# Optimization experiments

Hardware: AMD Instinct MI355X
Metric: run time of the kernel (lower is better)

## Reference

```python
import jax, jax.numpy as jnp
import numpy as np

B, M, N, D, H = 4, 8, 128, 32, 64
SMALL_V = 1e-8


def setup_inputs() -> dict:
    key = jax.random.key(0)
    ks = jax.random.split(key, 12)
    s = 0.05
    x = jax.random.normal(ks[0], (B, M, N, D), jnp.float32)
    sizes = jax.random.randint(ks[1], (B,), N // 2, N + 1)
    valid = (jnp.arange(N)[None, :] < sizes[:, None]).astype(jnp.float32)  # [B,N]
    x = x * valid[:, None, :, None]  # zero out padded items
    return {
        "x": x,
        "x_size": sizes.astype(jnp.float32),
        "W1a": jax.random.normal(ks[2], (D, 2 * D), jnp.float32) * s,
        "b1a": jax.random.normal(ks[3], (2 * D,), jnp.float32) * s,
        "W1b": jax.random.normal(ks[4], (2 * D, D), jnp.float32) * s,
        "b1b": jax.random.normal(ks[5], (D,), jnp.float32) * s,
        "W2a": jax.random.normal(ks[6], (D, 2 * D), jnp.float32) * s,
        "b2a": jax.random.normal(ks[7], (2 * D,), jnp.float32) * s,
        "W2b": jax.random.normal(ks[8], (2 * D, H), jnp.float32) * s,
        "b2b": jax.random.normal(ks[9], (H,), jnp.float32) * s,
        "w3": jax.random.normal(ks[10], (H,), jnp.float32) * s,
        "b3": jax.random.normal(ks[11], (1,), jnp.float32) * s,
    }


def _item_mask(x):
    # 1.0 where the item's feature row has any nonzero entry, else 0.0. [...,N,1]
    return jnp.any(x != 0, axis=-1, keepdims=True).astype(x.dtype)


def _set_norm(x, x_size):
    # layer_normalization with is_set_norm=True: normalize over (N*D) per set,
    # dividing by the true valid size x_size*D and masking padded items.
    b, m, n, d = x.shape
    mask = jnp.broadcast_to(_item_mask(x), x.shape).reshape(b, m, n * d)
    xr = x.reshape(b, m, n * d)
    denom = x_size[:, None] * d  # [B,1] -> broadcasts over nSet
    mean = jnp.sum(xr, axis=-1) / denom  # [B,M]
    diff = xr - mean[..., None]
    std = jnp.sqrt(jnp.sum(diff * diff * mask, axis=-1) / denom)  # [B,M]
    out = diff / (std[..., None] + SMALL_V) * mask
    return out.reshape(b, m, n, d)


def reference(x, x_size, W1a, b1a, W1b, b1b, W2a, b2a, W2b, b2b, w3, b3):
    mask = _item_mask(x)  # [B,M,N,1]
    x_orig = x
    xn = _set_norm(x, x_size) * mask  # [B,M,N,D]
    # MLP1 (rank-4 -> masked by its own input's item mask)
    m1 = _item_mask(xn)
    x1 = (jnp.matmul(jax.nn.gelu(jnp.matmul(xn, W1a) + b1a), W1b) + b1b) * m1
    # pairwise differences: x_diff[b,m,i,j,:] = x1[b,m,i,:] - xn[b,m,j,:]
    x_diff = x1[:, :, :, None, :] - xn[:, :, None, :, :]  # [B,M,N,N,D]
    # MLP2 (rank-5 -> no mask, is_SoftMax=0)
    e = jnp.matmul(jax.nn.gelu(jnp.matmul(x_diff, W2a) + b2a), W2b) + b2b  # [B,M,N,N,H]
    # aggregation: out[b,m,j,h,d] = sum_i e[b,m,i,j,h] * x1[b,m,i,d]
    agg = jnp.einsum('bmijh,bmid->bmjhd', e, x1)
    # MLP3_linear: Dense(1) over H, then squeeze
    out = jnp.einsum('bmjhd,h->bmjd', agg, w3) + b3[0]
    out = (out + x_orig) * mask
    return out
```

## Files before the change

### kernel.cpp

```cpp
#include <hip/hip_runtime.h>

#define BMC 32
#define NNC 128
#define DDC 32
#define KKC 64
constexpr int ND = NNC * DDC;
constexpr int NK = NNC * KKC;
#define SMALLV 1e-8f

__device__ __forceinline__ float gelu_f(float v) {
    float v2 = v * v;
    float p  = fmaf(0.1029432f, v2, 2.3022082f);
    float e  = __builtin_amdgcn_exp2f(v * p);
    float r  = __builtin_amdgcn_rcpf(e + 1.0f);
    return fmaf(-v, r, v);
}

__global__ __launch_bounds__(256) void mlp_kernel(
    const float* __restrict__ x, const float* __restrict__ x_size,
    const float* __restrict__ W1a, const float* __restrict__ b1a,
    const float* __restrict__ W1b, const float* __restrict__ b1b,
    const float* __restrict__ W2a, const float* __restrict__ b2a,
    const float* __restrict__ W2b, const float* __restrict__ b2b,
    const float* __restrict__ w3,
    float* __restrict__ x1g, float* __restrict__ A1g, float* __restrict__ A2t,
    float* __restrict__ v2g, float* __restrict__ c3g)
{
    __shared__ float sW1a[DDC * KKC];
    __shared__ float sW1b[KKC * DDC];
    __shared__ float sW2a[DDC * KKC];
    __shared__ float sXn[8 * DDC];
    __shared__ float sH[8 * KKC];
    __shared__ float sX1[8 * DDC];
    __shared__ float sB1a[KKC], sB2a[KKC], sB1b[DDC];
    __shared__ float sAny[NNC];
    __shared__ float sRed[4];

    const int t  = threadIdx.x;
    const int bm = blockIdx.x >> 4;
    const int nt = blockIdx.x & 15;
    const int n0 = nt * 8;
    const int w  = t >> 6;

    {
        const float4* a4 = (const float4*)W1a;
        const float4* b4 = (const float4*)W1b;
        const float4* c4 = (const float4*)W2a;
        float4* sa = (float4*)sW1a; float4* sb = (float4*)sW1b; float4* sc = (float4*)sW2a;
        sa[t] = a4[t]; sa[t + 256] = a4[t + 256];
        sb[t] = b4[t]; sb[t + 256] = b4[t + 256];
        sc[t] = c4[t]; sc[t + 256] = c4[t + 256];
    }
    if (t < KKC) { sB1a[t] = b1a[t]; sB2a[t] = b2a[t]; }
    if (t < DDC) { sB1b[t] = b1b[t]; }
    if (t < NNC) sAny[t] = 0.f;
    __syncthreads();

    const float4* xs4 = (const float4*)(x + (size_t)bm * ND);
    float4 v4[4];
    float lsum = 0.f;
    #pragma unroll
    for (int s = 0; s < 4; ++s) {
        int f = t + s * 256;
        float4 q = xs4[f];
        v4[s] = q;
        lsum += q.x + q.y + q.z + q.w;
        if (q.x != 0.f || q.y != 0.f || q.z != 0.f || q.w != 0.f) sAny[f >> 3] = 1.f;
    }
    #pragma unroll
    for (int off = 32; off; off >>= 1) lsum += __shfl_xor(lsum, off);
    if ((t & 63) == 0) sRed[w] = lsum;
    __syncthreads();
    const float denom = x_size[bm >> 3] * (float)DDC;
    const float mean  = (sRed[0] + sRed[1] + sRed[2] + sRed[3]) / denom;

    float lsq = 0.f;
    #pragma unroll
    for (int s = 0; s < 4; ++s) {
        int f = t + s * 256;
        float mk = sAny[f >> 3];
        float dx = v4[s].x - mean, dy = v4[s].y - mean;
        float dz = v4[s].z - mean, dw = v4[s].w - mean;
        lsq += mk * (dx * dx + dy * dy + dz * dz + dw * dw);
    }
    #pragma unroll
    for (int off = 32; off; off >>= 1) lsq += __shfl_xor(lsq, off);
    __syncthreads();
    if ((t & 63) == 0) sRed[w] = lsq;
    __syncthreads();
    const float sq  = sRed[0] + sRed[1] + sRed[2] + sRed[3];
    const float inv = 1.f / (sqrtf(sq / denom) + SMALLV);

    {
        float xv = x[(size_t)bm * ND + n0 * DDC + t];
        sXn[t] = (xv - mean) * inv * sAny[n0 + (t >> 5)];
    }
    __syncthreads();

    const int k = t & 63;

    #pragma unroll
    for (int r = 0; r < 2; ++r) {
        int n = w + r * 4;
        const float* xr = &sXn[n * DDC];
        float acc = sB1a[k];
        #pragma unroll
        for (int d = 0; d < DDC; ++d) acc = fmaf(xr[d], sW1a[d * KKC + k], acc);
        sH[n * KKC + k] = gelu_f(acc);
    }
    __syncthreads();

    {
        const int d2 = t & 31;
        const int n  = t >> 5;
        const float* hr = &sH[n * KKC];
        float acc = sB1b[d2];
        #pragma unroll
        for (int q = 0; q < KKC; ++q) acc = fmaf(hr[q], sW1b[q * DDC + d2], acc);
        float val = acc * sAny[n0 + n];
        sX1[n * DDC + d2] = val;
        x1g[(size_t)bm * ND + (n0 + n) * DDC + d2] = val;
    }
    __syncthreads();

    #pragma unroll
    for (int r = 0; r < 2; ++r) {
        int n = w + r * 4;
        const float* x1r = &sX1[n * DDC];
        const float* xnr = &sXn[n * DDC];
        float a1 = sB2a[k], a2 = 0.f;
        #pragma unroll
        for (int d = 0; d < DDC; ++d) {
            a1 = fmaf(x1r[d], sW2a[d * KKC + k], a1);
            a2 = fmaf(xnr[d], sW2a[d * KKC + k], a2);
        }
        A1g[(size_t)bm * NK + (n0 + n) * KKC + k] = a1;
        A2t[(size_t)bm * NK + k * NNC + (n0 + n)] = a2;
    }

    if (blockIdx.x == 0) {
        int kk = t >> 2, hq = t & 3;
        float p = 0.f;
        #pragma unroll
        for (int h = 0; h < 16; ++h)
            p = fmaf(W2b[kk * KKC + hq * 16 + h], w3[hq * 16 + h], p);
        __syncthreads();
        sH[t] = p;
        __syncthreads();
        if (hq == 0) v2g[kk] = sH[t] + sH[t + 1] + sH[t + 2] + sH[t + 3];
        if (t < 64) {
            float q = b2b[t] * w3[t];
            #pragma unroll
            for (int off = 32; off; off >>= 1) q += __shfl_xor(q, off);
            if (t == 0) c3g[0] = q;
        }
    }
}

__global__ __launch_bounds__(256) void pair_kernel(
    const float* __restrict__ x_size,
    const float* __restrict__ A1g, const float* __restrict__ A2t,
    const float* __restrict__ x1g, const float* __restrict__ v2g,
    const float* __restrict__ c3g, float* __restrict__ partial)
{
    __shared__ float sA2[KKC * 64];
    __shared__ float sA1[8 * KKC];
    __shared__ float sX1[8 * DDC];
    __shared__ float sS[8 * 64];
    __shared__ float sV2[KKC];

    const int t    = threadIdx.x;
    const int bm   = blockIdx.x >> 5;
    const int jg   = (blockIdx.x >> 4) & 1;
    const int ig   = blockIdx.x & 15;

    const int iN = (int)(x_size[bm >> 3] + 0.5f);
    if (ig * 8 >= iN || jg * 64 >= iN) return;

    const int wv   = t >> 6;
    const int lane = t & 63;

    {
        const float* A2b = A2t + (size_t)bm * NK + jg * 64;
        float4* s4 = (float4*)sA2;
        #pragma unroll
        for (int s = 0; s < 4; ++s) {
            int idx = t + s * 256;
            int k = idx >> 4, f = idx & 15;
            s4[idx] = *(const float4*)(A2b + k * NNC + f * 4);
        }
    }
    {
        const float2* a1s = (const float2*)(A1g + (size_t)bm * NK + ig * 8 * KKC);
        ((float2*)sA1)[t] = a1s[t];
        sX1[t] = x1g[(size_t)bm * ND + ig * 8 * DDC + t];
        if (t < KKC) sV2[t] = v2g[t];
    }
    const float c3 = c3g[0];
    __syncthreads();

    {
        const int i0 = wv * 2, i1 = i0 + 1;
        float S0 = c3, S1 = c3;
        #pragma unroll 8
        for (int k = 0; k < KKC; ++k) {
            float a2v = sA2[k * 64 + lane];
            float vk  = sV2[k];
            float a10 = sA1[i0 * KKC + k];
            float a11 = sA1[i1 * KKC + k];
            S0 = fmaf(gelu_f(a10 - a2v), vk, S0);
            S1 = fmaf(gelu_f(a11 - a2v), vk, S1);
        }
        sS[i0 * 64 + lane] = S0;
        sS[i1 * 64 + lane] = S1;
    }
    __syncthreads();

    {
        const int j  = t >> 2;
        const int dq = t & 3;
        float acc[8];
        #pragma unroll
        for (int d = 0; d < 8; ++d) acc[d] = 0.f;
        #pragma unroll
        for (int i = 0; i < 8; ++i) {
            float Sv = sS[i * 64 + j];
            const float4* xf = (const float4*)&sX1[i * DDC + dq * 8];
            float4 xa = xf[0], xb = xf[1];
            acc[0] = fmaf(Sv, xa.x, acc[0]);
            acc[1] = fmaf(Sv, xa.y, acc[1]);
            acc[2] = fmaf(Sv, xa.z, acc[2]);
            acc[3] = fmaf(Sv, xa.w, acc[3]);
            acc[4] = fmaf(Sv, xb.x, acc[4]);
            acc[5] = fmaf(Sv, xb.y, acc[5]);
            acc[6] = fmaf(Sv, xb.z, acc[6]);
            acc[7] = fmaf(Sv, xb.w, acc[7]);
        }
        float* pb = partial + ((size_t)((bm * 2 + jg) * 16 + ig)) * 2048 + t * 8;
        ((float4*)pb)[0] = make_float4(acc[0], acc[1], acc[2], acc[3]);
        ((float4*)pb)[1] = make_float4(acc[4], acc[5], acc[6], acc[7]);
    }
}

__global__ __launch_bounds__(256) void final_kernel(
    const float* __restrict__ x, const float* __restrict__ x_size,
    const float* __restrict__ b3,
    const float* __restrict__ partial, float* __restrict__ out)
{
    const int gid = blockIdx.x * 256 + threadIdx.x;
    const int bm  = gid >> 12;
    const int rem = gid & 4095;
    float xv = x[gid];
    unsigned long long bal = __ballot(xv != 0.f);
    int lane = threadIdx.x & 63;
    unsigned long long half = (lane < 32) ? (bal & 0xFFFFFFFFull) : (bal >> 32);
    if (half == 0ull) { out[gid] = 0.f; return; }

    const int iN  = (int)(x_size[bm >> 3] + 0.5f);
    const int nig = (iN + 7) >> 3;
    const int jgp = rem >> 11;
    const size_t pb = ((size_t)((bm * 2 + jgp) * 16)) * 2048 + (rem & 2047);
    float sum = 0.f;
    for (int ig = 0; ig < nig; ++ig) sum += partial[pb + (size_t)ig * 2048];
    out[gid] = sum + b3[0] + xv;
}

extern "C" void kernel_launch(void* const* d_in, const int* in_sizes, int n_in,
                              void* d_out, int out_size, void* d_ws, size_t ws_size,
                              hipStream_t stream) {
    const float* x      = (const float*)d_in[0];
    const float* x_size = (const float*)d_in[1];
    const float* W1a    = (const float*)d_in[2];
    const float* b1a    = (const float*)d_in[3];
    const float* W1b    = (const float*)d_in[4];
    const float* b1b    = (const float*)d_in[5];
    const float* W2a    = (const float*)d_in[6];
    const float* b2a    = (const float*)d_in[7];
    const float* W2b    = (const float*)d_in[8];
    const float* b2b    = (const float*)d_in[9];
    const float* w3     = (const float*)d_in[10];
    const float* b3     = (const float*)d_in[11];
    float* out = (float*)d_out;

    float* ws      = (float*)d_ws;
    float* x1g     = ws;
    float* A1g     = x1g + (size_t)BMC * ND;
    float* A2t     = A1g + (size_t)BMC * NK;
    float* v2g     = A2t + (size_t)BMC * NK;
    float* c3g     = v2g + KKC;
    float* partial = c3g + 64;

    mlp_kernel<<<BMC * 16, 256, 0, stream>>>(x, x_size,
        W1a, b1a, W1b, b1b, W2a, b2a, W2b, b2b, w3,
        x1g, A1g, A2t, v2g, c3g);
    pair_kernel<<<BMC * 32, 256, 0, stream>>>(x_size, A1g, A2t, x1g, v2g, c3g, partial);
    final_kernel<<<512, 256, 0, stream>>>(x, x_size, b3, partial, out);
}
```

Measured before the change: 103.7 us.

## Fuse three kernels into one cooperative kernel with grid-wide syncs

Replaces the three separate launches (MLP precompute, pairwise aggregation, final reduction) with a single cooperative kernel of 512 blocks that separates the phases with grid.sync(). Each block processes two pair tiles in the middle phase. The aim is to remove the launch overhead and inter-kernel gaps between the three stages. In exchange it depends on 2 blocks fitting per CU for co-residency and pays for grid barriers. It falls back to the old three-kernel path if the occupancy check or the cooperative launch fails.

Measured after the change: 249.4 us. 2.4x slower.

```diff
diff --git a/kernel.cpp b/kernel.cpp
--- a/kernel.cpp
+++ b/kernel.cpp
@@ -1,4 +1,7 @@
 #include <hip/hip_runtime.h>
+#include <hip/hip_cooperative_groups.h>
+
+namespace cg = cooperative_groups;
 
 #define BMC 32
 #define NNC 128
@@ -14,6 +17,266 @@
     float e  = __builtin_amdgcn_exp2f(v * p);
     float r  = __builtin_amdgcn_rcpf(e + 1.0f);
     return fmaf(-v, r, v);
+}
+
+__global__ __launch_bounds__(256, 2) void fused_kernel(
+    const float* __restrict__ x, const float* __restrict__ x_size,
+    const float* __restrict__ W1a, const float* __restrict__ b1a,
+    const float* __restrict__ W1b, const float* __restrict__ b1b,
+    const float* __restrict__ W2a, const float* __restrict__ b2a,
+    const float* __restrict__ W2b, const float* __restrict__ b2b,
+    const float* __restrict__ w3, const float* __restrict__ b3,
+    float* __restrict__ x1g, float* __restrict__ A1g, float* __restrict__ A2t,
+    float* __restrict__ v2g, float* __restrict__ c3g,
+    float* __restrict__ partial, float* __restrict__ out)
+{
+    __shared__ __align__(16) float smem[7680];
+
+    const int t   = threadIdx.x;
+    const int blk = blockIdx.x;
+    cg::grid_group grid = cg::this_grid();
+
+    {
+        float* sW1a = smem;
+        float* sW1b = smem + 2048;
+        float* sW2a = smem + 4096;
+        float* sXn  = smem + 6144;
+        float* sH   = smem + 6400;
+        float* sX1  = smem + 6912;
+        float* sB1a = smem + 7168;
+        float* sB2a = smem + 7232;
+        float* sB1b = smem + 7296;
+        float* sAny = smem + 7328;
+        float* sRed = smem + 7456;
+
+        const int bm = blk >> 4;
+        const int nt = blk & 15;
+        const int n0 = nt * 8;
+        const int w  = t >> 6;
+
+        {
+            const float4* a4 = (const float4*)W1a;
+            const float4* b4 = (const float4*)W1b;
+            const float4* c4 = (const float4*)W2a;
+            float4* sa = (float4*)sW1a; float4* sb = (float4*)sW1b; float4* sc = (float4*)sW2a;
+            sa[t] = a4[t]; sa[t + 256] = a4[t + 256];
+            sb[t] = b4[t]; sb[t + 256] = b4[t + 256];
+            sc[t] = c4[t]; sc[t + 256] = c4[t + 256];
+        }
+        if (t < KKC) { sB1a[t] = b1a[t]; sB2a[t] = b2a[t]; }
+        if (t < DDC) { sB1b[t] = b1b[t]; }
+        if (t < NNC) sAny[t] = 0.f;
+        __syncthreads();
+
+        const float4* xs4 = (const float4*)(x + (size_t)bm * ND);
+        float4 v4[4];
+        float lsum = 0.f;
+        #pragma unroll
+        for (int s = 0; s < 4; ++s) {
+            int f = t + s * 256;
+            float4 q = xs4[f];
+            v4[s] = q;
+            lsum += q.x + q.y + q.z + q.w;
+            if (q.x != 0.f || q.y != 0.f || q.z != 0.f || q.w != 0.f) sAny[f >> 3] = 1.f;
+        }
+        #pragma unroll
+        for (int off = 32; off; off >>= 1) lsum += __shfl_xor(lsum, off);
+        if ((t & 63) == 0) sRed[w] = lsum;
+        __syncthreads();
+        const float denom = x_size[bm >> 3] * (float)DDC;
+        const float mean  = (sRed[0] + sRed[1] + sRed[2] + sRed[3]) / denom;
+
+        float lsq = 0.f;
+        #pragma unroll
+        for (int s = 0; s < 4; ++s) {
+            int f = t + s * 256;
+            float mk = sAny[f >> 3];
+            float dx = v4[s].x - mean, dy = v4[s].y - mean;
+            float dz = v4[s].z - mean, dw = v4[s].w - mean;
+            lsq += mk * (dx * dx + dy * dy + dz * dz + dw * dw);
+        }
+        #pragma unroll
+        for (int off = 32; off; off >>= 1) lsq += __shfl_xor(lsq, off);
+        __syncthreads();
+        if ((t & 63) == 0) sRed[w] = lsq;
+        __syncthreads();
+        const float sq  = sRed[0] + sRed[1] + sRed[2] + sRed[3];
+        const float inv = 1.f / (sqrtf(sq / denom) + SMALLV);
+
+        {
+            float xv = x[(size_t)bm * ND + n0 * DDC + t];
+            sXn[t] = (xv - mean) * inv * sAny[n0 + (t >> 5)];
+        }
+        __syncthreads();
+
+        const int k = t & 63;
+
+        #pragma unroll
+        for (int r = 0; r < 2; ++r) {
+            int n = w + r * 4;
+            const float* xr = &sXn[n * DDC];
+            float acc = sB1a[k];
+            #pragma unroll
+            for (int d = 0; d < DDC; ++d) acc = fmaf(xr[d], sW1a[d * KKC + k], acc);
+            sH[n * KKC + k] = gelu_f(acc);
+        }
+        __syncthreads();
+
+        {
+            const int d2 = t & 31;
+            const int n  = t >> 5;
+            const float* hr = &sH[n * KKC];
+            float acc = sB1b[d2];
+            #pragma unroll
+            for (int q = 0; q < KKC; ++q) acc = fmaf(hr[q], sW1b[q * DDC + d2], acc);
+            float val = acc * sAny[n0 + n];
+            sX1[n * DDC + d2] = val;
+            x1g[(size_t)bm * ND + (n0 + n) * DDC + d2] = val;
+        }
+        __syncthreads();
+
+        #pragma unroll
+        for (int r = 0; r < 2; ++r) {
+            int n = w + r * 4;
+            const float* x1r = &sX1[n * DDC];
+            const float* xnr = &sXn[n * DDC];
+            float a1 = sB2a[k], a2 = 0.f;
+            #pragma unroll
+            for (int d = 0; d < DDC; ++d) {
+                a1 = fmaf(x1r[d], sW2a[d * KKC + k], a1);
+                a2 = fmaf(xnr[d], sW2a[d * KKC + k], a2);
+            }
+            A1g[(size_t)bm * NK + (n0 + n) * KKC + k] = a1;
+            A2t[(size_t)bm * NK + k * NNC + (n0 + n)] = a2;
+        }
+
+        if (blk == 0) {
+            int kk = t >> 2, hq = t & 3;
+            float p = 0.f;
+            #pragma unroll
+            for (int h = 0; h < 16; ++h)
+                p = fmaf(W2b[kk * KKC + hq * 16 + h], w3[hq * 16 + h], p);
+            __syncthreads();
+            sH[t] = p;
+            __syncthreads();
+            if (hq == 0) v2g[kk] = sH[t] + sH[t + 1] + sH[t + 2] + sH[t + 3];
+            if (t < 64) {
+                float q = b2b[t] * w3[t];
+                #pragma unroll
+                for (int off = 32; off; off >>= 1) q += __shfl_xor(q, off);
+                if (t == 0) c3g[0] = q;
+            }
+        }
+    }
+
+    grid.sync();
+
+    {
+        float* sA2 = smem;
+        float* sA1 = smem + 4096;
+        float* sX1 = smem + 4608;
+        float* sS  = smem + 4864;
+        float* sV2 = smem + 5376;
+
+        #pragma unroll
+        for (int rep = 0; rep < 2; ++rep) {
+            const int tile = blk + rep * 512;
+            const int bm = tile >> 5;
+            const int jg = (tile >> 4) & 1;
+            const int ig = tile & 15;
+
+            const int iN = (int)(x_size[bm >> 3] + 0.5f);
+            const bool active = (ig * 8 < iN) && (jg * 64 < iN);
+
+            if (active) {
+                const int wv   = t >> 6;
+                const int lane = t & 63;
+
+                {
+                    const float* A2b = A2t + (size_t)bm * NK + jg * 64;
+                    float4* s4 = (float4*)sA2;
+                    #pragma unroll
+                    for (int s = 0; s < 4; ++s) {
+                        int idx = t + s * 256;
+                        int kk = idx >> 4, f = idx & 15;
+                        s4[idx] = *(const float4*)(A2b + kk * NNC + f * 4);
+                    }
+                }
+                {
+                    const float2* a1s = (const float2*)(A1g + (size_t)bm * NK + ig * 8 * KKC);
+                    ((float2*)sA1)[t] = a1s[t];
+                    sX1[t] = x1g[(size_t)bm * ND + ig * 8 * DDC + t];
+                    if (t < KKC) sV2[t] = v2g[t];
+                }
+                const float c3 = c3g[0];
+                __syncthreads();
+
+                {
+                    const int i0 = wv * 2, i1 = i0 + 1;
+                    float S0 = c3, S1 = c3;
+                    #pragma unroll 8
+                    for (int k = 0; k < KKC; ++k) {
+                        float a2v = sA2[k * 64 + lane];
+                        float vk  = sV2[k];
+                        float a10 = sA1[i0 * KKC + k];
+                        float a11 = sA1[i1 * KKC + k];
+                        S0 = fmaf(gelu_f(a10 - a2v), vk, S0);
+                        S1 = fmaf(gelu_f(a11 - a2v), vk, S1);
+                    }
+                    sS[i0 * 64 + lane] = S0;
+                    sS[i1 * 64 + lane] = S1;
+                }
+                __syncthreads();
+
+                {
+                    const int j  = t >> 2;
+                    const int dq = t & 3;
+                    float acc[8];
+                    #pragma unroll
+                    for (int d = 0; d < 8; ++d) acc[d] = 0.f;
+                    #pragma unroll
+                    for (int i = 0; i < 8; ++i) {
+                        float Sv = sS[i * 64 + j];
+                        const float4* xf = (const float4*)&sX1[i * DDC + dq * 8];
+                        float4 xa = xf[0], xb = xf[1];
+                        acc[0] = fmaf(Sv, xa.x, acc[0]);
+                        acc[1] = fmaf(Sv, xa.y, acc[1]);
+                        acc[2] = fmaf(Sv, xa.z, acc[2]);
+                        acc[3] = fmaf(Sv, xa.w, acc[3]);
+                        acc[4] = fmaf(Sv, xb.x, acc[4]);
+                        acc[5] = fmaf(Sv, xb.y, acc[5]);
+                        acc[6] = fmaf(Sv, xb.z, acc[6]);
+                        acc[7] = fmaf(Sv, xb.w, acc[7]);
+                    }
+                    float* pb = partial + ((size_t)((bm * 2 + jg) * 16 + ig)) * 2048 + t * 8;
+                    ((float4*)pb)[0] = make_float4(acc[0], acc[1], acc[2], acc[3]);
+                    ((float4*)pb)[1] = make_float4(acc[4], acc[5], acc[6], acc[7]);
+                }
+            }
+            if (rep == 0) __syncthreads();
+        }
+    }
+
+    grid.sync();
+
+    {
+        const int gid = blk * 256 + t;
+        const int bm  = gid >> 12;
+        const int rem = gid & 4095;
+        float xv = x[gid];
+        unsigned long long bal = __ballot(xv != 0.f);
+        int lane = t & 63;
+        unsigned long long half = (lane < 32) ? (bal & 0xFFFFFFFFull) : (bal >> 32);
+        if (half == 0ull) { out[gid] = 0.f; return; }
+
+        const int iN  = (int)(x_size[bm >> 3] + 0.5f);
+        const int nig = (iN + 7) >> 3;
+        const int jgp = rem >> 11;
+        const size_t pb = ((size_t)((bm * 2 + jgp) * 16)) * 2048 + (rem & 2047);
+        float sum = 0.f;
+        for (int ig = 0; ig < nig; ++ig) sum += partial[pb + (size_t)ig * 2048];
+        out[gid] = sum + b3[0] + xv;
+    }
 }
 
 __global__ __launch_bounds__(256) void mlp_kernel(
@@ -290,6 +553,29 @@
     float* c3g     = v2g + KKC;
     float* partial = c3g + 64;
 
+    static int use_coop = -1;
+    if (use_coop < 0) {
+        int nb = 0;
+        hipError_t e = hipOccupancyMaxActiveBlocksPerMultiprocessor(
+            &nb, (const void*)fused_kernel, 256, 0);
+        use_coop = (e == hipSuccess && nb >= 2) ? 1 : 0;
+    }
+
+    if (use_coop) {
+        void* args[] = {
+            (void*)&x, (void*)&x_size,
+            (void*)&W1a, (void*)&b1a, (void*)&W1b, (void*)&b1b,
+            (void*)&W2a, (void*)&b2a, (void*)&W2b, (void*)&b2b,
+            (void*)&w3, (void*)&b3,
+            (void*)&x1g, (void*)&A1g, (void*)&A2t, (void*)&v2g, (void*)&c3g,
+            (void*)&partial, (void*)&out
+        };
+        hipError_t e = hipLaunchCooperativeKernel((const void*)fused_kernel,
+                                                  dim3(512), dim3(256), args, 0, stream);
+        if (e == hipSuccess) return;
+        use_coop = 0;
+    }
+
     mlp_kernel<<<BMC * 16, 256, 0, stream>>>(x, x_size,
         W1a, b1a, W1b, b1b, W2a, b2a, W2b, b2b, w3,
         x1g, A1g, A2t, v2g, c3g);
```

## Fuse MLP, pairwise and final kernels into one per-set j-tile kernel

Applied to the files above, without the earlier changes.

Replaces the three-kernel pipeline with one kernel where each block owns a set and a 16-wide j tile. Each block recomputes set norm, MLP1 and A1 for the whole set in shared memory, with weights held in registers. It then does the pairwise GELU reduction and aggregation locally, writing the output directly. This removes global workspace round-trips, partial-sum reduction and two launches, at the cost of redundant MLP1 work across the 8 j-tile blocks and only 256 blocks with high register and LDS use.

Measured after the change: 106.9 us. 1.03x slower.

```diff
diff --git a/kernel.cpp b/kernel.cpp
--- a/kernel.cpp
+++ b/kernel.cpp
@@ -1,11 +1,9 @@
 #include <hip/hip_runtime.h>
 
-#define BMC 32
 #define NNC 128
 #define DDC 32
 #define KKC 64
 constexpr int ND = NNC * DDC;
-constexpr int NK = NNC * KKC;
 #define SMALLV 1e-8f
 
 __device__ __forceinline__ float gelu_f(float v) {
@@ -16,44 +14,69 @@
     return fmaf(-v, r, v);
 }
 
-__global__ __launch_bounds__(256) void mlp_kernel(
+__global__ __launch_bounds__(256, 1) void fused2(
     const float* __restrict__ x, const float* __restrict__ x_size,
     const float* __restrict__ W1a, const float* __restrict__ b1a,
     const float* __restrict__ W1b, const float* __restrict__ b1b,
     const float* __restrict__ W2a, const float* __restrict__ b2a,
     const float* __restrict__ W2b, const float* __restrict__ b2b,
-    const float* __restrict__ w3,
-    float* __restrict__ x1g, float* __restrict__ A1g, float* __restrict__ A2t,
-    float* __restrict__ v2g, float* __restrict__ c3g)
+    const float* __restrict__ w3, const float* __restrict__ b3,
+    float* __restrict__ out)
 {
-    __shared__ float sW1a[DDC * KKC];
-    __shared__ float sW1b[KKC * DDC];
-    __shared__ float sW2a[DDC * KKC];
-    __shared__ float sXn[8 * DDC];
-    __shared__ float sH[8 * KKC];
-    __shared__ float sX1[8 * DDC];
-    __shared__ float sB1a[KKC], sB2a[KKC], sB1b[DDC];
-    __shared__ float sAny[NNC];
-    __shared__ float sRed[4];
-
-    const int t  = threadIdx.x;
-    const int bm = blockIdx.x >> 4;
-    const int nt = blockIdx.x & 15;
-    const int n0 = nt * 8;
-    const int w  = t >> 6;
+    __shared__ __align__(16) float smem[16384];
+
+    const int t   = threadIdx.x;
+    const int blk = blockIdx.x;
+    const int bm  = blk >> 3;
+    const int jt  = blk & 7;
+    const int k   = t & 63;
+    const int w   = t >> 6;
+    const int dL  = t & 31;
+
+    const int iN = (int)(x_size[bm >> 3] + 0.5f);
+
+    float* sX1  = smem;
+    float* sA1  = smem + 4096;
+    float* sXn  = smem + 4096;
+    float* sH32 = smem + 8192;
+    float* scr  = smem + 8192;
+    float* sA2  = smem + 12416;
+    float* sS   = smem + 13568;
+    float* sV2  = smem + 15872;
+    float* sAny = smem + 15936;
+    float* sRed = smem + 16064;
+    float* sC3  = smem + 16072;
+
+    if (jt * 16 >= iN) {
+        ((float2*)(out + (size_t)bm * ND + jt * 512))[t] = make_float2(0.f, 0.f);
+        return;
+    }
+
+    float colA[32];
+    #pragma unroll
+    for (int d = 0; d < 32; ++d) colA[d] = W1a[d * 64 + k];
+    float colB[64];
+    #pragma unroll
+    for (int q = 0; q < 64; ++q) colB[q] = W1b[q * 32 + dL];
+    const float rb1a = b1a[k];
+    const float rb1b = b1b[dL];
+    const float rb2a = b2a[k];
 
     {
-        const float4* a4 = (const float4*)W1a;
-        const float4* b4 = (const float4*)W1b;
-        const float4* c4 = (const float4*)W2a;
-        float4* sa = (float4*)sW1a; float4* sb = (float4*)sW1b; float4* sc = (float4*)sW2a;
-        sa[t] = a4[t]; sa[t + 256] = a4[t + 256];
-        sb[t] = b4[t]; sb[t + 256] = b4[t + 256];
-        sc[t] = c4[t]; sc[t + 256] = c4[t + 256];
-    }
-    if (t < KKC) { sB1a[t] = b1a[t]; sB2a[t] = b2a[t]; }
-    if (t < DDC) { sB1b[t] = b1b[t]; }
-    if (t < NNC) sAny[t] = 0.f;
+        const int kk = t >> 2, hq = t & 3;
+        float p = 0.f;
+        #pragma unroll
+        for (int h = 0; h < 16; ++h)
+            p = fmaf(W2b[kk * 64 + hq * 16 + h], w3[hq * 16 + h], p);
+        scr[t] = p;
+    }
+    if (t < 64) {
+        float q = b2b[t] * w3[t];
+        #pragma unroll
+        for (int off = 32; off; off >>= 1) q += __shfl_xor(q, off);
+        if (t == 0) sC3[0] = q;
+    }
+    if (t < 128) sAny[t] = 0.f;
     __syncthreads();
 
     const float4* xs4 = (const float4*)(x + (size_t)bm * ND);
@@ -71,9 +94,10 @@
     for (int off = 32; off; off >>= 1) lsum += __shfl_xor(lsum, off);
     if ((t & 63) == 0) sRed[w] = lsum;
     __syncthreads();
-    const float denom = x_size[bm >> 3] * (float)DDC;
+    if ((t & 3) == 0)
+        sV2[t >> 2] = scr[t] + scr[t + 1] + scr[t + 2] + scr[t + 3];
+    const float denom = x_size[bm >> 3] * 32.f;
     const float mean  = (sRed[0] + sRed[1] + sRed[2] + sRed[3]) / denom;
-
     float lsq = 0.f;
     #pragma unroll
     for (int s = 0; s < 4; ++s) {
@@ -91,183 +115,159 @@
     const float sq  = sRed[0] + sRed[1] + sRed[2] + sRed[3];
     const float inv = 1.f / (sqrtf(sq / denom) + SMALLV);
 
+    #pragma unroll
+    for (int s = 0; s < 4; ++s) {
+        int f = t + s * 256;
+        float mk = sAny[f >> 3] * inv;
+        float4 q = v4[s];
+        q.x = (q.x - mean) * mk; q.y = (q.y - mean) * mk;
+        q.z = (q.z - mean) * mk; q.w = (q.w - mean) * mk;
+        ((float4*)sXn)[f] = q;
+    }
+    __syncthreads();
+
+    for (int c = 0; c < 4; ++c) {
+        const int rb = c * 32;
+        const bool live = (rb < iN);
+        if (live) {
+            #pragma unroll
+            for (int r = 0; r < 8; ++r) {
+                const int nl = w + 4 * r;
+                const float4* xr4 = (const float4*)&sXn[(rb + nl) * 32];
+                float acc = rb1a;
+                #pragma unroll
+                for (int dq = 0; dq < 8; ++dq) {
+                    float4 xv = xr4[dq];
+                    acc = fmaf(xv.x, colA[4 * dq + 0], acc);
+                    acc = fmaf(xv.y, colA[4 * dq + 1], acc);
+                    acc = fmaf(xv.z, colA[4 * dq + 2], acc);
+                    acc = fmaf(xv.w, colA[4 * dq + 3], acc);
+                }
+                sH32[nl * 64 + k] = gelu_f(acc);
+            }
+        }
+        __syncthreads();
+        if (live) {
+            #pragma unroll
+            for (int p = 0; p < 4; ++p) {
+                const int nl = (t >> 5) + 8 * p;
+                const float4* hr4 = (const float4*)&sH32[nl * 64];
+                float acc = rb1b;
+                #pragma unroll
+                for (int qq = 0; qq < 16; ++qq) {
+                    float4 hv = hr4[qq];
+                    acc = fmaf(hv.x, colB[4 * qq + 0], acc);
+                    acc = fmaf(hv.y, colB[4 * qq + 1], acc);
+                    acc = fmaf(hv.z, colB[4 * qq + 2], acc);
+                    acc = fmaf(hv.w, colB[4 * qq + 3], acc);
+                }
+                sX1[(rb + nl) * 32 + dL] = acc * sAny[rb + nl];
+            }
+        } else {
+            #pragma unroll
+            for (int p = 0; p < 4; ++p)
+                sX1[(rb + (t >> 5) + 8 * p) * 32 + dL] = 0.f;
+        }
+        __syncthreads();
+    }
+
+    float colC[32];
+    #pragma unroll
+    for (int d = 0; d < 32; ++d) colC[d] = W2a[d * 64 + k];
+    #pragma unroll
+    for (int q = 0; q < 4; ++q) {
+        const int jl = w + 4 * q;
+        const float4* xr4 = (const float4*)&sXn[(jt * 16 + jl) * 32];
+        float acc = 0.f;
+        #pragma unroll
+        for (int dq = 0; dq < 8; ++dq) {
+            float4 xv = xr4[dq];
+            acc = fmaf(xv.x, colC[4 * dq + 0], acc);
+            acc = fmaf(xv.y, colC[4 * dq + 1], acc);
+            acc = fmaf(xv.z, colC[4 * dq + 2], acc);
+            acc = fmaf(xv.w, colC[4 * dq + 3], acc);
+        }
+        sA2[k * 18 + jl] = acc;
+    }
+    __syncthreads();
+
+    const int ICAP = (iN + 3) & ~3;
+    for (int n = w; n < ICAP; n += 4) {
+        const float4* x14 = (const float4*)&sX1[n * 32];
+        float acc = rb2a;
+        #pragma unroll
+        for (int dq = 0; dq < 8; ++dq) {
+            float4 xv = x14[dq];
+            acc = fmaf(xv.x, colC[4 * dq + 0], acc);
+            acc = fmaf(xv.y, colC[4 * dq + 1], acc);
+            acc = fmaf(xv.z, colC[4 * dq + 2], acc);
+            acc = fmaf(xv.w, colC[4 * dq + 3], acc);
+        }
+        sA1[n * 65 + k] = acc;
+    }
+    __syncthreads();
+
+    const float c3 = sC3[0];
     {
-        float xv = x[(size_t)bm * ND + n0 * DDC + t];
-        sXn[t] = (xv - mean) * inv * sAny[n0 + (t >> 5)];
-    }
-    __syncthreads();
-
-    const int k = t & 63;
-
-    #pragma unroll
-    for (int r = 0; r < 2; ++r) {
-        int n = w + r * 4;
-        const float* xr = &sXn[n * DDC];
-        float acc = sB1a[k];
-        #pragma unroll
-        for (int d = 0; d < DDC; ++d) acc = fmaf(xr[d], sW1a[d * KKC + k], acc);
-        sH[n * KKC + k] = gelu_f(acc);
+        const int jp = t & 7;
+        const int ic = t >> 3;
+        const int i0 = ic * 4;
+        if (i0 < iN) {
+            float a0x = c3, a0y = c3, a1x = c3, a1y = c3;
+            float a2x = c3, a2y = c3, a3x = c3, a3y = c3;
+            #pragma unroll 4
+            for (int kk = 0; kk < 64; ++kk) {
+                const float2 a2v = *(const float2*)&sA2[kk * 18 + 2 * jp];
+                const float vk  = sV2[kk];
+                const float* a1p = &sA1[i0 * 65 + kk];
+                const float b0 = a1p[0];
+                const float b1 = a1p[65];
+                const float b2 = a1p[130];
+                const float b3r = a1p[195];
+                a0x = fmaf(gelu_f(b0 - a2v.x), vk, a0x);
+                a0y = fmaf(gelu_f(b0 - a2v.y), vk, a0y);
+                a1x = fmaf(gelu_f(b1 - a2v.x), vk, a1x);
+                a1y = fmaf(gelu_f(b1 - a2v.y), vk, a1y);
+                a2x = fmaf(gelu_f(b2 - a2v.x), vk, a2x);
+                a2y = fmaf(gelu_f(b2 - a2v.y), vk, a2y);
+                a3x = fmaf(gelu_f(b3r - a2v.x), vk, a3x);
+                a3y = fmaf(gelu_f(b3r - a2v.y), vk, a3y);
+            }
+            *(float2*)&sS[(i0 + 0) * 18 + 2 * jp] = make_float2(a0x, a0y);
+            *(float2*)&sS[(i0 + 1) * 18 + 2 * jp] = make_float2(a1x, a1y);
+            *(float2*)&sS[(i0 + 2) * 18 + 2 * jp] = make_float2(a2x, a2y);
+            *(float2*)&sS[(i0 + 3) * 18 + 2 * jp] = make_float2(a3x, a3y);
+        }
     }
     __syncthreads();
 
     {
-        const int d2 = t & 31;
-        const int n  = t >> 5;
-        const float* hr = &sH[n * KKC];
-        float acc = sB1b[d2];
-        #pragma unroll
-        for (int q = 0; q < KKC; ++q) acc = fmaf(hr[q], sW1b[q * DDC + d2], acc);
-        float val = acc * sAny[n0 + n];
-        sX1[n * DDC + d2] = val;
-        x1g[(size_t)bm * ND + (n0 + n) * DDC + d2] = val;
-    }
-    __syncthreads();
-
-    #pragma unroll
-    for (int r = 0; r < 2; ++r) {
-        int n = w + r * 4;
-        const float* x1r = &sX1[n * DDC];
-        const float* xnr = &sXn[n * DDC];
-        float a1 = sB2a[k], a2 = 0.f;
-        #pragma unroll
-        for (int d = 0; d < DDC; ++d) {
-            a1 = fmaf(x1r[d], sW2a[d * KKC + k], a1);
-            a2 = fmaf(xnr[d], sW2a[d * KKC + k], a2);
-        }
-        A1g[(size_t)bm * NK + (n0 + n) * KKC + k] = a1;
-        A2t[(size_t)bm * NK + k * NNC + (n0 + n)] = a2;
-    }
-
-    if (blockIdx.x == 0) {
-        int kk = t >> 2, hq = t & 3;
-        float p = 0.f;
-        #pragma unroll
-        for (int h = 0; h < 16; ++h)
-            p = fmaf(W2b[kk * KKC + hq * 16 + h], w3[hq * 16 + h], p);
-        __syncthreads();
-        sH[t] = p;
-        __syncthreads();
-        if (hq == 0) v2g[kk] = sH[t] + sH[t + 1] + sH[t + 2] + sH[t + 3];
-        if (t < 64) {
-            float q = b2b[t] * w3[t];
-            #pragma unroll
-            for (int off = 32; off; off >>= 1) q += __shfl_xor(q, off);
-            if (t == 0) c3g[0] = q;
-        }
-    }
-}
-
-__global__ __launch_bounds__(256) void pair_kernel(
-    const float* __restrict__ x_size,
-    const float* __restrict__ A1g, const float* __restrict__ A2t,
-    const float* __restrict__ x1g, const float* __restrict__ v2g,
-    const float* __restrict__ c3g, float* __restrict__ partial)
-{
-    __shared__ float sA2[KKC * 64];
-    __shared__ float sA1[8 * KKC];
-    __shared__ float sX1[8 * DDC];
-    __shared__ float sS[8 * 64];
-    __shared__ float sV2[KKC];
-
-    const int t    = threadIdx.x;
-    const int bm   = blockIdx.x >> 5;
-    const int jg   = (blockIdx.x >> 4) & 1;
-    const int ig   = blockIdx.x & 15;
-
-    const int iN = (int)(x_size[bm >> 3] + 0.5f);
-    if (ig * 8 >= iN || jg * 64 >= iN) return;
-
-    const int wv   = t >> 6;
-    const int lane = t & 63;
-
-    {
-        const float* A2b = A2t + (size_t)bm * NK + jg * 64;
-        float4* s4 = (float4*)sA2;
-        #pragma unroll
-        for (int s = 0; s < 4; ++s) {
-            int idx = t + s * 256;
-            int k = idx >> 4, f = idx & 15;
-            s4[idx] = *(const float4*)(A2b + k * NNC + f * 4);
-        }
-    }
-    {
-        const float2* a1s = (const float2*)(A1g + (size_t)bm * NK + ig * 8 * KKC);
-        ((float2*)sA1)[t] = a1s[t];
-        sX1[t] = x1g[(size_t)bm * ND + ig * 8 * DDC + t];
-        if (t < KKC) sV2[t] = v2g[t];
-    }
-    const float c3 = c3g[0];
-    __syncthreads();
-
-    {
-        const int i0 = wv * 2, i1 = i0 + 1;
-        float S0 = c3, S1 = c3;
-        #pragma unroll 8
-        for (int k = 0; k < KKC; ++k) {
-            float a2v = sA2[k * 64 + lane];
-            float vk  = sV2[k];
-            float a10 = sA1[i0 * KKC + k];
-            float a11 = sA1[i1 * KKC + k];
-            S0 = fmaf(gelu_f(a10 - a2v), vk, S0);
-            S1 = fmaf(gelu_f(a11 - a2v), vk, S1);
-        }
-        sS[i0 * 64 + lane] = S0;
-        sS[i1 * 64 + lane] = S1;
-    }
-    __syncthreads();
-
-    {
-        const int j  = t >> 2;
-        const int dq = t & 3;
-        float acc[8];
-        #pragma unroll
-        for (int d = 0; d < 8; ++d) acc[d] = 0.f;
-        #pragma unroll
-        for (int i = 0; i < 8; ++i) {
-            float Sv = sS[i * 64 + j];
-            const float4* xf = (const float4*)&sX1[i * DDC + dq * 8];
-            float4 xa = xf[0], xb = xf[1];
-            acc[0] = fmaf(Sv, xa.x, acc[0]);
-            acc[1] = fmaf(Sv, xa.y, acc[1]);
-            acc[2] = fmaf(Sv, xa.z, acc[2]);
-            acc[3] = fmaf(Sv, xa.w, acc[3]);
-            acc[4] = fmaf(Sv, xb.x, acc[4]);
-            acc[5] = fmaf(Sv, xb.y, acc[5]);
-            acc[6] = fmaf(Sv, xb.z, acc[6]);
-            acc[7] = fmaf(Sv, xb.w, acc[7]);
-        }
-        float* pb = partial + ((size_t)((bm * 2 + jg) * 16 + ig)) * 2048 + t * 8;
-        ((float4*)pb)[0] = make_float4(acc[0], acc[1], acc[2], acc[3]);
-        ((float4*)pb)[1] = make_float4(acc[4], acc[5], acc[6], acc[7]);
-    }
-}
-
-__global__ __launch_bounds__(256) void final_kernel(
-    const float* __restrict__ x, const float* __restrict__ x_size,
-    const float* __restrict__ b3,
-    const float* __restrict__ partial, float* __restrict__ out)
-{
-    const int gid = blockIdx.x * 256 + threadIdx.x;
-    const int bm  = gid >> 12;
-    const int rem = gid & 4095;
-    float xv = x[gid];
-    unsigned long long bal = __ballot(xv != 0.f);
-    int lane = threadIdx.x & 63;
-    unsigned long long half = (lane < 32) ? (bal & 0xFFFFFFFFull) : (bal >> 32);
-    if (half == 0ull) { out[gid] = 0.f; return; }
-
-    const int iN  = (int)(x_size[bm >> 3] + 0.5f);
-    const int nig = (iN + 7) >> 3;
-    const int jgp = rem >> 11;
-    const size_t pb = ((size_t)((bm * 2 + jgp) * 16)) * 2048 + (rem & 2047);
-    float sum = 0.f;
-    for (int ig = 0; ig < nig; ++ig) sum += partial[pb + (size_t)ig * 2048];
-    out[gid] = sum + b3[0] + xv;
+        const int j  = t >> 4;
+        const int d0 = (t & 15) * 2;
+        const int jg = jt * 16 + j;
+        float s0 = 0.f, s1 = 0.f;
+        #pragma unroll 4
+        for (int i = 0; i < ICAP; ++i) {
+            const float Sv = sS[i * 18 + j];
+            const float2 xv = *(const float2*)&sX1[i * 32 + d0];
+            s0 = fmaf(Sv, xv.x, s0);
+            s1 = fmaf(Sv, xv.y, s1);
+        }
+        const float msk = sAny[jg];
+        const float b3v = b3[0];
+        const size_t ob = (size_t)bm * ND + jg * 32 + d0;
+        const float2 xo = *(const float2*)&x[ob];
+        float2 o;
+        o.x = (s0 + b3v + xo.x) * msk;
+        o.y = (s1 + b3v + xo.y) * msk;
+        *(float2*)&out[ob] = o;
+    }
 }
 
 extern "C" void kernel_launch(void* const* d_in, const int* in_sizes, int n_in,
                               void* d_out, int out_size, void* d_ws, size_t ws_size,
                               hipStream_t stream) {
+    (void)in_sizes; (void)n_in; (void)d_ws; (void)ws_size; (void)out_size;
     const float* x      = (const float*)d_in[0];
     const float* x_size = (const float*)d_in[1];
     const float* W1a    = (const float*)d_in[2];
@@ -282,17 +282,6 @@
     const float* b3     = (const float*)d_in[11];
     float* out = (float*)d_out;
 
-    float* ws      = (float*)d_ws;
-    float* x1g     = ws;
-    float* A1g     = x1g + (size_t)BMC * ND;
-    float* A2t     = A1g + (size_t)BMC * NK;
-    float* v2g     = A2t + (size_t)BMC * NK;
-    float* c3g     = v2g + KKC;
-    float* partial = c3g + 64;
-
-    mlp_kernel<<<BMC * 16, 256, 0, stream>>>(x, x_size,
-        W1a, b1a, W1b, b1b, W2a, b2a, W2b, b2b, w3,
-        x1g, A1g, A2t, v2g, c3g);
-    pair_kernel<<<BMC * 32, 256, 0, stream>>>(x_size, A1g, A2t, x1g, v2g, c3g, partial);
-    final_kernel<<<512, 256, 0, stream>>>(x, x_size, b3, partial, out);
+    fused2<<<dim3(256), dim3(256), 0, stream>>>(
+        x, x_size, W1a, b1a, W1b, b1b, W2a, b2a, W2b, b2b, w3, b3, out);
 }
```
